# Optimization experiments

Measured on AMD Instinct MI355X. Metric: run time of the kernel, lower is better.

## Reference

```python
import jax, jax.numpy as jnp
import numpy as np

NUM_HEADS = 8
NUM_LAYER = 4


def setup_inputs() -> dict:
    key = jax.random.key(0)
    k1, k2, k3, k4, k5, k6, k7 = jax.random.split(key, 7)
    bs, num, C = 2, 2048, 256
    H0 = (jax.random.uniform(k1, (bs, num, num)) < 0.3).astype(jnp.float32)
    vertex_feat = jax.random.normal(k2, (bs, C, num), dtype=jnp.float32)
    edge_feat = jax.random.normal(k3, (bs, C, num), dtype=jnp.float32)
    s = 1.0 / np.sqrt(C)
    # Conv1d(kernel_size=1) weights, squeezed to [C_out, C_in]
    Wq = jax.random.uniform(k4, (C, C), minval=-s, maxval=s, dtype=jnp.float32)
    bq = jax.random.uniform(k5, (C,), minval=-s, maxval=s, dtype=jnp.float32)
    Wk = jax.random.uniform(k6, (C, C), minval=-s, maxval=s, dtype=jnp.float32)
    bk = jax.random.uniform(k7, (C,), minval=-s, maxval=s, dtype=jnp.float32)
    return {"H0": H0, "vertex_feat": vertex_feat, "edge_feat": edge_feat,
            "Wq": Wq, "bq": bq, "Wk": Wk, "bk": bk, "iter": 1}


def reference(H0, vertex_feat, edge_feat, Wq, bq, Wk, bk, iter):
    bs, num, _ = H0.shape
    C = vertex_feat.shape[1]
    h = NUM_HEADS
    d = C // h
    # 1x1 Conv1d == per-position linear; reshape to heads: [bs, h, d, num]
    Q = (jnp.einsum('oc,bcn->bon', Wq, vertex_feat) + bq[None, :, None]).reshape(bs, h, d, num)
    K = (jnp.einsum('oc,bcn->bon', Wk, edge_feat) + bk[None, :, None]).reshape(bs, h, d, num)
    attn = jnp.einsum('bhco,bhci->bhoi', Q, K) / np.sqrt(d)  # [bs, h, num, num]
    # attention_mask = (1 - H0).masked_fill((1-H0).bool(), -1e9)
    m = 1.0 - H0
    m = jnp.where(m != 0, jnp.float32(-1e9), m)
    score = jax.nn.sigmoid(attn + m[:, None, :, :]).sum(axis=1) / h  # [bs, num, num]
    # top-k row thresholding (k static: iter is a python int)
    k = max(1, round(num * 0.1 * (NUM_LAYER - 1 - iter)))
    topk_vals = jax.lax.top_k(score, k)[0]           # sorted descending
    a_min = topk_vals[..., -1:]                      # row-wise k-th largest
    W = jnp.where(score >= a_min, score, jnp.float32(0.0))
    H = jnp.where(W > 0, H0, jnp.float32(0.0))
    # degree normalizations (1e-10 keeps them finite; torch isinf branch is a no-op)
    De_n_1 = (1.0 / (H.sum(axis=1) + 1e-10))[..., None]  # [bs, num, 1]
    Dv_n_1 = (1.0 / (H.sum(axis=2) + 1e-10))[..., None]  # [bs, num, 1]
    # F.normalize(W.sum(dim=1), dim=1): L2 normalize with eps=1e-12
    W_edge = W.sum(axis=1)
    W_edge = W_edge / jnp.maximum(jnp.linalg.norm(W_edge, axis=1, keepdims=True), 1e-12)
    W_edge = W_edge[..., None]  # [bs, num, 1]
    return (H, W, De_n_1, Dv_n_1, W_edge)
```

## Files before the change

### kernel.cpp

```cpp
#include <hip/hip_runtime.h>
#include <math.h>

#define NUM 2048
#define CDIM 256
#define NUM_LAYER 4

typedef short bf16x8 __attribute__((ext_vector_type(8)));
typedef unsigned short u16x8 __attribute__((ext_vector_type(8)));
typedef float f32x4 __attribute__((ext_vector_type(4)));

static __device__ __forceinline__ unsigned short f2bf(float f) {
  unsigned u = __float_as_uint(f);
  unsigned r = 0x7FFFu + ((u >> 16) & 1u);
  return (unsigned short)((u + r) >> 16);
}
static __device__ __forceinline__ float bf2f(unsigned short h) {
  return __uint_as_float(((unsigned)h) << 16);
}

__global__ __launch_bounds__(256) void proj_kernel(
    const float* __restrict__ Wq, const float* __restrict__ bq,
    const float* __restrict__ Wk, const float* __restrict__ bk,
    const float* __restrict__ vf, const float* __restrict__ ef,
    unsigned short* __restrict__ Qhi, unsigned short* __restrict__ Qmd,
    unsigned short* __restrict__ Qlo, unsigned short* __restrict__ Khi,
    unsigned short* __restrict__ Kmd, unsigned short* __restrict__ Klo)
{
  const int z = blockIdx.z;
  const int b = z >> 1, mm2 = z & 1;
  const float* __restrict__ Wmat = mm2 ? Wk : Wq;
  const float* __restrict__ bias = mm2 ? bk : bq;
  const float* __restrict__ x = (mm2 ? ef : vf) + (size_t)b * CDIM * NUM;
  unsigned short* __restrict__ ohi = mm2 ? Khi : Qhi;
  unsigned short* __restrict__ omd = mm2 ? Kmd : Qmd;
  unsigned short* __restrict__ olo = mm2 ? Klo : Qlo;

  const int n0 = blockIdx.x * 64;
  const int o0 = blockIdx.y * 64;
  __shared__ float Xs[32][65];
  __shared__ float Ws[64][33];
  __shared__ float T[64][69];
  const int t = threadIdx.x;
  const int tx = t & 15, ty = t >> 4;

  float acc[4][4];
  #pragma unroll
  for (int a = 0; a < 4; a++)
    #pragma unroll
    for (int c = 0; c < 4; c++) acc[a][c] = 0.0f;

  for (int cc = 0; cc < CDIM; cc += 32) {
    #pragma unroll
    for (int e = 0; e < 2; e++) {
      int f = t * 2 + e;
      int row = f >> 4, c4 = f & 15;
      const float4 v = *(const float4*)(&x[(size_t)(cc + row) * NUM + n0 + c4 * 4]);
      Xs[row][c4*4+0] = v.x; Xs[row][c4*4+1] = v.y;
      Xs[row][c4*4+2] = v.z; Xs[row][c4*4+3] = v.w;
    }
    #pragma unroll
    for (int e = 0; e < 2; e++) {
      int f = t * 2 + e;
      int row = f >> 3, c4 = f & 7;
      const float4 v = *(const float4*)(&Wmat[(size_t)(o0 + row) * CDIM + cc + c4 * 4]);
      Ws[row][c4*4+0] = v.x; Ws[row][c4*4+1] = v.y;
      Ws[row][c4*4+2] = v.z; Ws[row][c4*4+3] = v.w;
    }
    __syncthreads();
    #pragma unroll
    for (int kk = 0; kk < 32; kk++) {
      float xv[4], wv[4];
      #pragma unroll
      for (int j = 0; j < 4; j++) xv[j] = Xs[kk][tx*4+j];
      #pragma unroll
      for (int j = 0; j < 4; j++) wv[j] = Ws[ty*4+j][kk];
      #pragma unroll
      for (int oi = 0; oi < 4; oi++)
        #pragma unroll
        for (int ni = 0; ni < 4; ni++)
          acc[oi][ni] = fmaf(wv[oi], xv[ni], acc[oi][ni]);
    }
    __syncthreads();
  }
  float bb[4];
  #pragma unroll
  for (int oi = 0; oi < 4; oi++) bb[oi] = bias[o0 + ty*4 + oi];
  #pragma unroll
  for (int ni = 0; ni < 4; ni++)
    #pragma unroll
    for (int oi = 0; oi < 4; oi++)
      T[tx*4+ni][ty*4+oi] = acc[oi][ni] + bb[oi];
  __syncthreads();
  const int n_l = t >> 2;
  const int oc  = (t & 3) * 16;
  float xv[16];
  #pragma unroll
  for (int j = 0; j < 16; j++) xv[j] = T[n_l][oc + j];
  unsigned short hi[16], md[16], lo[16];
  #pragma unroll
  for (int j = 0; j < 16; j++) {
    unsigned short h = f2bf(xv[j]);
    float r1 = xv[j] - bf2f(h);
    unsigned short mdj = f2bf(r1);
    float r2 = r1 - bf2f(mdj);
    hi[j] = h; md[j] = mdj; lo[j] = f2bf(r2);
  }
  const size_t gb = ((size_t)b * NUM + n0 + n_l) * CDIM + o0 + oc;
  *(u16x8*)&ohi[gb]   = *(u16x8*)&hi[0];
  *(u16x8*)&ohi[gb+8] = *(u16x8*)&hi[8];
  *(u16x8*)&omd[gb]   = *(u16x8*)&md[0];
  *(u16x8*)&omd[gb+8] = *(u16x8*)&md[8];
  *(u16x8*)&olo[gb]   = *(u16x8*)&lo[0];
  *(u16x8*)&olo[gb+8] = *(u16x8*)&lo[8];
}

__global__ __launch_bounds__(512, 2) void score_kernel(
    const unsigned short* __restrict__ Qhi, const unsigned short* __restrict__ Qmd,
    const unsigned short* __restrict__ Qlo, const unsigned short* __restrict__ Khi,
    const unsigned short* __restrict__ Kmd, const unsigned short* __restrict__ Klo,
    const float* __restrict__ H0, float* __restrict__ score)
{
  const int b = blockIdx.z;
  const int i0 = blockIdx.x * 128;
  const int o0 = blockIdx.y * 128;
  const int t = threadIdx.x, lane = t & 63, wave = t >> 6;
  const int m = lane & 15, quad = lane >> 4;
  const int obl = (wave & 1) * 64;
  const int ibl = (wave >> 1) * 32;

  __shared__ unsigned short qsh[3][128][36];
  __shared__ unsigned short ksh[3][128][36];

  const int srow = t >> 2;
  const int schk = (t & 3) * 8;

  f32x4 ssum[4][2];
  #pragma unroll
  for (int a = 0; a < 4; a++)
    #pragma unroll
    for (int c = 0; c < 2; c++) ssum[a][c] = (f32x4){0.f, 0.f, 0.f, 0.f};

  const float SC = -1.4426950408889634f * 0.17677669529663687f;

  u16x8 pq[3], pk[3];
  {
    const size_t go = ((size_t)b * NUM + o0 + srow) * CDIM + schk;
    const size_t gi = ((size_t)b * NUM + i0 + srow) * CDIM + schk;
    pq[0] = *(const u16x8*)&Qhi[go];
    pq[1] = *(const u16x8*)&Qmd[go];
    pq[2] = *(const u16x8*)&Qlo[go];
    pk[0] = *(const u16x8*)&Khi[gi];
    pk[1] = *(const u16x8*)&Kmd[gi];
    pk[2] = *(const u16x8*)&Klo[gi];
  }

  for (int h = 0; h < 8; h++) {
    __syncthreads();
    #pragma unroll
    for (int cp = 0; cp < 3; cp++) {
      *(u16x8*)&qsh[cp][srow][schk] = pq[cp];
      *(u16x8*)&ksh[cp][srow][schk] = pk[cp];
    }
    __syncthreads();
    if (h < 7) {
      const int coff = (h + 1) * 32;
      const size_t go = ((size_t)b * NUM + o0 + srow) * CDIM + coff + schk;
      const size_t gi = ((size_t)b * NUM + i0 + srow) * CDIM + coff + schk;
      pq[0] = *(const u16x8*)&Qhi[go];
      pq[1] = *(const u16x8*)&Qmd[go];
      pq[2] = *(const u16x8*)&Qlo[go];
      pk[0] = *(const u16x8*)&Khi[gi];
      pk[1] = *(const u16x8*)&Kmd[gi];
      pk[2] = *(const u16x8*)&Klo[gi];
    }
    bf16x8 a[4][3];
    #pragma unroll
    for (int ot = 0; ot < 4; ot++)
      #pragma unroll
      for (int cp = 0; cp < 3; cp++)
        a[ot][cp] = *(const bf16x8*)&qsh[cp][obl + ot*16 + m][quad*8];
    #pragma unroll
    for (int it = 0; it < 2; it++) {
      const bf16x8 b0 = *(const bf16x8*)&ksh[0][ibl + it*16 + m][quad*8];
      const bf16x8 b1 = *(const bf16x8*)&ksh[1][ibl + it*16 + m][quad*8];
      const bf16x8 b2 = *(const bf16x8*)&ksh[2][ibl + it*16 + m][quad*8];
      #pragma unroll
      for (int ot = 0; ot < 4; ot++) {
        f32x4 c = (f32x4){0.f, 0.f, 0.f, 0.f};
        c = __builtin_amdgcn_mfma_f32_16x16x32_bf16(a[ot][0], b0, c, 0, 0, 0);
        c = __builtin_amdgcn_mfma_f32_16x16x32_bf16(a[ot][0], b1, c, 0, 0, 0);
        c = __builtin_amdgcn_mfma_f32_16x16x32_bf16(a[ot][1], b0, c, 0, 0, 0);
        c = __builtin_amdgcn_mfma_f32_16x16x32_bf16(a[ot][1], b1, c, 0, 0, 0);
        c = __builtin_amdgcn_mfma_f32_16x16x32_bf16(a[ot][0], b2, c, 0, 0, 0);
        c = __builtin_amdgcn_mfma_f32_16x16x32_bf16(a[ot][2], b0, c, 0, 0, 0);
        #pragma unroll
        for (int r = 0; r < 4; r++)
          ssum[ot][it][r] += __builtin_amdgcn_rcpf(1.0f + __builtin_amdgcn_exp2f(c[r] * SC));
      }
    }
  }
  const int ob = o0 + obl, ib = i0 + ibl;
  #pragma unroll
  for (int ot = 0; ot < 4; ot++)
    #pragma unroll
    for (int it = 0; it < 2; it++)
      #pragma unroll
      for (int r = 0; r < 4; r++) {
        const int row = ob + ot*16 + quad*4 + r;
        const int col = ib + it*16 + m;
        const size_t idx = ((size_t)b * NUM + row) * NUM + col;
        score[idx] = H0[idx] * ssum[ot][it][r] * 0.125f;
      }
}

__global__ __launch_bounds__(256) void topk_apply_kernel(
    float* __restrict__ scoreW, float* __restrict__ Hout,
    const int* __restrict__ iterp, float* __restrict__ DvOut)
{
  const int row = blockIdx.x;
  __shared__ unsigned int hist[4][256];
  __shared__ unsigned int cum[257];
  __shared__ unsigned int s_sel, s_rem;
  __shared__ float red[4];
  const int t = threadIdx.x;
  const int wid = t >> 6, lane = t & 63;
  unsigned int* __restrict__ srow = (unsigned int*)scoreW + (size_t)row * NUM;

  const uint4 va = ((const uint4*)srow)[t*2];
  const uint4 vb = ((const uint4*)srow)[t*2+1];
  unsigned int v[8] = {va.x, va.y, va.z, va.w, vb.x, vb.y, vb.z, vb.w};

  const int it = iterp[0];
  int k = (int)((double)NUM * 0.1 * (double)(NUM_LAYER - 1 - it) + 0.5);
  if (k < 1) k = 1;
  if (k > NUM) k = NUM;

  unsigned int prefix = 0;
  unsigned int rem = (unsigned int)k;
  unsigned int* hflat = &hist[0][0];

  for (int pass = 3; pass >= 0; pass--) {
    const int shift = pass * 8;
    const unsigned int pmask = (pass == 3) ? 0u : (0xFFFFFFFFu << (shift + 8));
    #pragma unroll
    for (int j = 0; j < 4; j++) hflat[t + 256*j] = 0;
    __syncthreads();
    unsigned int zc = 0;
    #pragma unroll
    for (int j = 0; j < 8; j++) {
      unsigned int val = v[j];
      if ((val & pmask) == prefix) {
        unsigned int bin = (val >> shift) & 255u;
        if (bin) atomicAdd(&hist[wid][bin], 1u);
        else zc++;
      }
    }
    #pragma unroll
    for (int off = 32; off > 0; off >>= 1) zc += __shfl_down(zc, off, 64);
    if (lane == 0 && zc) atomicAdd(&hist[wid][0], zc);
    __syncthreads();
    if (t < 64) {
      unsigned int T[4], s[4];
      #pragma unroll
      for (int q = 0; q < 4; q++)
        T[q] = hist[0][t*4+q] + hist[1][t*4+q] + hist[2][t*4+q] + hist[3][t*4+q];
      s[3] = T[3];
      s[2] = T[2] + s[3];
      s[1] = T[1] + s[2];
      s[0] = T[0] + s[1];
      unsigned int tot = s[0];
      #pragma unroll
      for (int off = 1; off < 64; off <<= 1) {
        unsigned int y = __shfl_down(tot, off, 64);
        if (lane + off < 64) tot += y;
      }
      const unsigned int above_chunk = tot - s[0];
      #pragma unroll
      for (int q = 0; q < 4; q++) cum[t*4+q] = s[q] + above_chunk;
      if (t == 0) cum[256] = 0;
    }
    __syncthreads();
    unsigned int c = cum[t], above = cum[t + 1];
    if (c >= rem && above < rem) { s_sel = (unsigned int)t; s_rem = rem - above; }
    __syncthreads();
    prefix |= (s_sel << shift);
    rem = s_rem;
    __syncthreads();
  }

  const unsigned int amin = prefix;
  float* __restrict__ Hrow = Hout + (size_t)row * NUM;
  unsigned int w[8];
  float hh[8];
  float cnt = 0.0f;
  #pragma unroll
  for (int j = 0; j < 8; j++) {
    w[j] = (v[j] >= amin) ? v[j] : 0u;
    hh[j] = (w[j] != 0u) ? 1.0f : 0.0f;
    cnt += hh[j];
  }
  ((uint4*)srow)[t*2]   = make_uint4(w[0], w[1], w[2], w[3]);
  ((uint4*)srow)[t*2+1] = make_uint4(w[4], w[5], w[6], w[7]);
  ((float4*)Hrow)[t*2]   = make_float4(hh[0], hh[1], hh[2], hh[3]);
  ((float4*)Hrow)[t*2+1] = make_float4(hh[4], hh[5], hh[6], hh[7]);
  #pragma unroll
  for (int off = 32; off > 0; off >>= 1) cnt += __shfl_down(cnt, off, 64);
  if (lane == 0) red[wid] = cnt;
  __syncthreads();
  if (t == 0) {
    float tot = red[0] + red[1] + red[2] + red[3];
    DvOut[row] = 1.0f / (tot + 1e-10f);
  }
}

__global__ __launch_bounds__(256) void colsum_kernel(
    const float* __restrict__ Wmat,
    float* __restrict__ colH, float* __restrict__ colW)
{
  const int b = blockIdx.z;
  const int i = blockIdx.x * 256 + threadIdx.x;
  const int o0 = blockIdx.y * 128;
  float sh = 0.0f, sw = 0.0f;
  for (int o = 0; o < 128; o++) {
    size_t idx = ((size_t)b * NUM + o0 + o) * NUM + i;
    float w = Wmat[idx];
    sw += w;
    sh += (w > 0.0f) ? 1.0f : 0.0f;
  }
  atomicAdd(&colH[b * NUM + i], sh);
  atomicAdd(&colW[b * NUM + i], sw);
}

__global__ __launch_bounds__(1024) void finalize_kernel(
    const float* __restrict__ colH, const float* __restrict__ colW,
    float* __restrict__ De, float* __restrict__ We)
{
  const int b = blockIdx.x;
  const int t = threadIdx.x;
  float cw[2];
  float sq = 0.0f;
  #pragma unroll
  for (int j = 0; j < 2; j++) {
    int i = t + 1024*j;
    float ch = colH[b * NUM + i];
    De[b * NUM + i] = 1.0f / (ch + 1e-10f);
    cw[j] = colW[b * NUM + i];
    sq += cw[j] * cw[j];
  }
  for (int off = 32; off > 0; off >>= 1) sq += __shfl_down(sq, off, 64);
  __shared__ float red[16];
  __shared__ float s_nrm;
  if ((t & 63) == 0) red[t >> 6] = sq;
  __syncthreads();
  if (t == 0) {
    float tot = 0.0f;
    for (int i2 = 0; i2 < 16; i2++) tot += red[i2];
    s_nrm = fmaxf(sqrtf(tot), 1e-12f);
  }
  __syncthreads();
  #pragma unroll
  for (int j = 0; j < 2; j++)
    We[b * NUM + t + 1024*j] = cw[j] / s_nrm;
}

extern "C" void kernel_launch(void* const* d_in, const int* in_sizes, int n_in,
                              void* d_out, int out_size, void* d_ws, size_t ws_size,
                              hipStream_t stream) {
  const float* H0 = (const float*)d_in[0];
  const float* vf = (const float*)d_in[1];
  const float* ef = (const float*)d_in[2];
  const float* Wq = (const float*)d_in[3];
  const float* bq = (const float*)d_in[4];
  const float* Wk = (const float*)d_in[5];
  const float* bk = (const float*)d_in[6];
  const int* iter = (const int*)d_in[7];

  float* out = (float*)d_out;
  const size_t nH = (size_t)2 * NUM * NUM;
  float* Hout  = out;
  float* Wout  = out + nH;
  float* DeOut = out + 2 * nH;
  float* DvOut = DeOut + 2 * NUM;
  float* WeOut = DvOut + 2 * NUM;

  float* colH = (float*)d_ws;
  float* colW = colH + 2 * NUM;

  const size_t nC = (size_t)2 * NUM * CDIM;
  unsigned short* base = (unsigned short*)Hout;
  unsigned short* Qhi = base;
  unsigned short* Qmd = base + nC;
  unsigned short* Qlo = base + 2 * nC;
  unsigned short* Khi = base + 3 * nC;
  unsigned short* Kmd = base + 4 * nC;
  unsigned short* Klo = base + 5 * nC;

  hipMemsetAsync(d_ws, 0, (size_t)2 * 2 * NUM * sizeof(float), stream);

  proj_kernel<<<dim3(NUM/64, CDIM/64, 4), 256, 0, stream>>>(
      Wq, bq, Wk, bk, vf, ef, Qhi, Qmd, Qlo, Khi, Kmd, Klo);
  score_kernel<<<dim3(NUM/128, NUM/128, 2), 512, 0, stream>>>(
      Qhi, Qmd, Qlo, Khi, Kmd, Klo, H0, Wout);
  topk_apply_kernel<<<dim3(2 * NUM), 256, 0, stream>>>(Wout, Hout, iter, DvOut);
  colsum_kernel<<<dim3(NUM/256, NUM/128, 2), 256, 0, stream>>>(Wout, colH, colW);
  finalize_kernel<<<dim3(2), 1024, 0, stream>>>(colH, colW, DeOut, WeOut);
}
```

Measured before the change: 206.4 us.

## Process one top-k row per wavefront and split colsum over more blocks

The top-k radix select now gives each 64-lane wavefront its own row and private histogram, so the block-wide __syncthreads barriers are gone. The bin search uses a ballot and shuffle inside the wave instead of shared cum arrays. Each lane keeps 32 values in registers, which raises register pressure. Separately, colsum blocks cover 64 rows instead of 128, which doubles the block count and the number of atomics to raise parallelism.

```diff
diff --git a/kernel.cpp b/kernel.cpp
--- a/kernel.cpp
+++ b/kernel.cpp
@@ -217,18 +217,16 @@
     float* __restrict__ scoreW, float* __restrict__ Hout,
     const int* __restrict__ iterp, float* __restrict__ DvOut)
 {
-  const int row = blockIdx.x;
-  __shared__ unsigned int hist[4][256];
-  __shared__ unsigned int cum[257];
-  __shared__ unsigned int s_sel, s_rem;
-  __shared__ float red[4];
-  const int t = threadIdx.x;
-  const int wid = t >> 6, lane = t & 63;
+  const int wave = threadIdx.x >> 6, lane = threadIdx.x & 63;
+  const int row = blockIdx.x * 4 + wave;
+  __shared__ unsigned int hist_all[4][256];
+  unsigned int* __restrict__ h = hist_all[wave];
   unsigned int* __restrict__ srow = (unsigned int*)scoreW + (size_t)row * NUM;
-
-  const uint4 va = ((const uint4*)srow)[t*2];
-  const uint4 vb = ((const uint4*)srow)[t*2+1];
-  unsigned int v[8] = {va.x, va.y, va.z, va.w, vb.x, vb.y, vb.z, vb.w};
+  float* __restrict__ Hrow = Hout + (size_t)row * NUM;
+
+  uint4 v[8];
+  #pragma unroll
+  for (int q = 0; q < 8; q++) v[q] = ((const uint4*)srow)[lane + 64*q];
 
   const int it = iterp[0];
   int k = (int)((double)NUM * 0.1 * (double)(NUM_LAYER - 1 - it) + 0.5);
@@ -237,80 +235,76 @@
 
   unsigned int prefix = 0;
   unsigned int rem = (unsigned int)k;
-  unsigned int* hflat = &hist[0][0];
 
   for (int pass = 3; pass >= 0; pass--) {
     const int shift = pass * 8;
     const unsigned int pmask = (pass == 3) ? 0u : (0xFFFFFFFFu << (shift + 8));
-    #pragma unroll
-    for (int j = 0; j < 4; j++) hflat[t + 256*j] = 0;
-    __syncthreads();
+    *(uint4*)&h[lane*4] = make_uint4(0u, 0u, 0u, 0u);
+    __threadfence_block();
     unsigned int zc = 0;
     #pragma unroll
-    for (int j = 0; j < 8; j++) {
-      unsigned int val = v[j];
-      if ((val & pmask) == prefix) {
-        unsigned int bin = (val >> shift) & 255u;
-        if (bin) atomicAdd(&hist[wid][bin], 1u);
-        else zc++;
+    for (int q = 0; q < 8; q++) {
+      const unsigned int vv[4] = {v[q].x, v[q].y, v[q].z, v[q].w};
+      #pragma unroll
+      for (int e = 0; e < 4; e++) {
+        unsigned int val = vv[e];
+        if ((val & pmask) == prefix) {
+          unsigned int bin = (val >> shift) & 255u;
+          if (bin) atomicAdd(&h[bin], 1u);
+          else zc++;
+        }
       }
     }
     #pragma unroll
     for (int off = 32; off > 0; off >>= 1) zc += __shfl_down(zc, off, 64);
-    if (lane == 0 && zc) atomicAdd(&hist[wid][0], zc);
-    __syncthreads();
-    if (t < 64) {
-      unsigned int T[4], s[4];
-      #pragma unroll
-      for (int q = 0; q < 4; q++)
-        T[q] = hist[0][t*4+q] + hist[1][t*4+q] + hist[2][t*4+q] + hist[3][t*4+q];
-      s[3] = T[3];
-      s[2] = T[2] + s[3];
-      s[1] = T[1] + s[2];
-      s[0] = T[0] + s[1];
-      unsigned int tot = s[0];
-      #pragma unroll
-      for (int off = 1; off < 64; off <<= 1) {
-        unsigned int y = __shfl_down(tot, off, 64);
-        if (lane + off < 64) tot += y;
-      }
-      const unsigned int above_chunk = tot - s[0];
-      #pragma unroll
-      for (int q = 0; q < 4; q++) cum[t*4+q] = s[q] + above_chunk;
-      if (t == 0) cum[256] = 0;
-    }
-    __syncthreads();
-    unsigned int c = cum[t], above = cum[t + 1];
-    if (c >= rem && above < rem) { s_sel = (unsigned int)t; s_rem = rem - above; }
-    __syncthreads();
-    prefix |= (s_sel << shift);
-    rem = s_rem;
-    __syncthreads();
+    if (lane == 0) h[0] = zc;
+    __threadfence_block();
+    const uint4 T = *(const uint4*)&h[lane*4];
+    unsigned int s3 = T.w;
+    unsigned int s2 = T.z + s3;
+    unsigned int s1 = T.y + s2;
+    unsigned int s0 = T.x + s1;
+    unsigned int tot = s0;
+    #pragma unroll
+    for (int off = 1; off < 64; off <<= 1) {
+      unsigned int y = __shfl_down(tot, off, 64);
+      if (lane + off < 64) tot += y;
+    }
+    const unsigned int ac = tot - s0;
+    const unsigned int cum[4]   = {s0 + ac, s1 + ac, s2 + ac, s3 + ac};
+    const unsigned int above[4] = {s1 + ac, s2 + ac, s3 + ac, ac};
+    int fq = -1;
+    #pragma unroll
+    for (int q = 0; q < 4; q++)
+      if (cum[q] >= rem && above[q] < rem) fq = q;
+    const unsigned long long mask = __ballot(fq >= 0);
+    const int src = (int)(__ffsll((long long)mask) - 1);
+    const unsigned int selbin = (fq >= 0) ? (unsigned int)(lane*4 + fq) : 0u;
+    const unsigned int nrem   = (fq >= 0) ? (rem - above[fq]) : 0u;
+    const unsigned int sel = (unsigned int)__shfl((int)selbin, src, 64);
+    rem = (unsigned int)__shfl((int)nrem, src, 64);
+    prefix |= (sel << shift);
   }
 
   const unsigned int amin = prefix;
-  float* __restrict__ Hrow = Hout + (size_t)row * NUM;
-  unsigned int w[8];
-  float hh[8];
   float cnt = 0.0f;
   #pragma unroll
-  for (int j = 0; j < 8; j++) {
-    w[j] = (v[j] >= amin) ? v[j] : 0u;
-    hh[j] = (w[j] != 0u) ? 1.0f : 0.0f;
-    cnt += hh[j];
-  }
-  ((uint4*)srow)[t*2]   = make_uint4(w[0], w[1], w[2], w[3]);
-  ((uint4*)srow)[t*2+1] = make_uint4(w[4], w[5], w[6], w[7]);
-  ((float4*)Hrow)[t*2]   = make_float4(hh[0], hh[1], hh[2], hh[3]);
-  ((float4*)Hrow)[t*2+1] = make_float4(hh[4], hh[5], hh[6], hh[7]);
+  for (int q = 0; q < 8; q++) {
+    unsigned int w0 = (v[q].x >= amin) ? v[q].x : 0u;
+    unsigned int w1 = (v[q].y >= amin) ? v[q].y : 0u;
+    unsigned int w2 = (v[q].z >= amin) ? v[q].z : 0u;
+    unsigned int w3 = (v[q].w >= amin) ? v[q].w : 0u;
+    float h0 = (w0 != 0u) ? 1.0f : 0.0f;
+    float h1 = (w1 != 0u) ? 1.0f : 0.0f;
+    float h2 = (w2 != 0u) ? 1.0f : 0.0f;
+    float h3 = (w3 != 0u) ? 1.0f : 0.0f;
+    cnt += h0 + h1 + h2 + h3;
+    ((uint4*)srow)[lane + 64*q] = make_uint4(w0, w1, w2, w3);
+    ((float4*)Hrow)[lane + 64*q] = make_float4(h0, h1, h2, h3);
+  }
   #pragma unroll
   for (int off = 32; off > 0; off >>= 1) cnt += __shfl_down(cnt, off, 64);
-  if (lane == 0) red[wid] = cnt;
-  __syncthreads();
-  if (t == 0) {
-    float tot = red[0] + red[1] + red[2] + red[3];
-    DvOut[row] = 1.0f / (tot + 1e-10f);
-  }
+  if (lane == 0) DvOut[row] = 1.0f / (cnt + 1e-10f);
 }
 
 __global__ __launch_bounds__(256) void colsum_kernel(
@@ -319,9 +313,9 @@
 {
   const int b = blockIdx.z;
   const int i = blockIdx.x * 256 + threadIdx.x;
-  const int o0 = blockIdx.y * 128;
+  const int o0 = blockIdx.y * 64;
   float sh = 0.0f, sw = 0.0f;
-  for (int o = 0; o < 128; o++) {
+  for (int o = 0; o < 64; o++) {
     size_t idx = ((size_t)b * NUM + o0 + o) * NUM + i;
     float w = Wmat[idx];
     sw += w;
@@ -401,7 +395,7 @@
       Wq, bq, Wk, bk, vf, ef, Qhi, Qmd, Qlo, Khi, Kmd, Klo);
   score_kernel<<<dim3(NUM/128, NUM/128, 2), 512, 0, stream>>>(
       Qhi, Qmd, Qlo, Khi, Kmd, Klo, H0, Wout);
-  topk_apply_kernel<<<dim3(2 * NUM), 256, 0, stream>>>(Wout, Hout, iter, DvOut);
-  colsum_kernel<<<dim3(NUM/256, NUM/128, 2), 256, 0, stream>>>(Wout, colH, colW);
+  topk_apply_kernel<<<dim3(NUM/2), 256, 0, stream>>>(Wout, Hout, iter, DvOut);
+  colsum_kernel<<<dim3(NUM/256, NUM/64, 2), 256, 0, stream>>>(Wout, colH, colW);
   finalize_kernel<<<dim3(2), 1024, 0, stream>>>(colH, colW, DeOut, WeOut);
 }
```

Result: faster. 200.3 us (-2.9%).
